# Kernel optimization log

Hardware: AMD Instinct MI355X
Metric: run time of the kernel (lower is better)

Reference implementation:

```python
import jax, jax.numpy as jnp
import numpy as np

VOCAB, D, E, B, S = 32000, 1024, 4, 4, 1024
DF = 4 * D  # Expert.internal_dim = d_model * 4


def setup_inputs() -> dict:
    key = jax.random.key(0)
    ks = jax.random.split(key, 14)
    sc = 0.02
    return {
        "tokens": jax.random.randint(ks[0], (B, S), 0, VOCAB),
        "emb": jax.random.normal(ks[1], (VOCAB, D), jnp.float32) * sc,
        "Wih": jax.random.normal(ks[2], (D, D), jnp.float32) * sc,
        "bih": jnp.zeros((D,), jnp.float32),
        "Whh": jax.random.normal(ks[3], (D, D), jnp.float32) * sc,
        "bhh": jnp.zeros((D,), jnp.float32),
        "Wg": jax.random.normal(ks[4], (E, D), jnp.float32) * sc,
        "W1": jax.random.normal(ks[5], (E, D, DF), jnp.float32) * sc,
        "b1": jnp.zeros((E, DF), jnp.float32),
        "W2": jax.random.normal(ks[6], (E, DF, D), jnp.float32) * sc,
        "b2": jnp.zeros((E, D), jnp.float32),
        "Wfc": jax.random.normal(ks[7], (VOCAB, D), jnp.float32) * sc,
        "bfc": jnp.zeros((VOCAB,), jnp.float32),
    }


def reference(tokens, emb, Wih, bih, Whh, bhh, Wg, W1, b1, W2, b2, Wfc, bfc):
    # token embedding: [B,S,D]
    x = emb[tokens]

    # nn.RNN(batch_first=True), tanh nonlinearity, h0 = zeros (h=None path)
    def step(h, xt):
        h = jnp.tanh(xt @ Wih.T + bih + h @ Whh.T + bhh)
        return h, h

    h0 = jnp.zeros((x.shape[0], x.shape[-1]), x.dtype)
    h_last, hs = jax.lax.scan(step, h0, jnp.swapaxes(x, 0, 1))  # hs: [S,B,D]
    x = jnp.swapaxes(hs, 0, 1)  # [B,S,D]

    # DarwinianRouter on pooled sequence repr: softmax gate, top_k=1
    gates = jax.nn.softmax(x.mean(axis=1) @ Wg.T, axis=-1)  # [B,E]
    w, idx = jax.lax.top_k(gates, 1)  # [B,1] each
    idx0 = idx[:, 0]

    # OuroborosMoE dispatch: per-sequence top-1 expert MLP, scaled by gate weight.
    # Gather per-batch expert params instead of boolean-mask gather/scatter loop.
    W1g, b1g = W1[idx0], b1[idx0]          # [B,D,DF], [B,DF]
    W2g, b2g = W2[idx0], b2[idx0]          # [B,DF,D], [B,D]
    h1 = jax.nn.gelu(jnp.einsum('bsd,bdf->bsf', x, W1g) + b1g[:, None, :], approximate=False)
    y = (jnp.einsum('bsf,bfd->bsd', h1, W2g) + b2g[:, None, :]) * w[:, :, None]  # [B,S,D]

    logits = y @ Wfc.T + bfc  # [B,S,VOCAB]
    return logits


if __name__ == "__main__":
    out = reference(**setup_inputs())
    print(out.shape)
```

## Files before the change

### kernel.cpp

```cpp
#include <hip/hip_runtime.h>
#include <hip/hip_bf16.h>
#include <math.h>

#define DD    1024
#define SS    1024
#define BB    4
#define EE    4
#define DFF   4096
#define VOC   32000

typedef __attribute__((ext_vector_type(8))) short v8s;
typedef __attribute__((ext_vector_type(4))) float v4f;

__device__ __forceinline__ unsigned short f2b(float f) {
    unsigned u = __float_as_uint(f);
    unsigned r = (u + 0x7FFFu + ((u >> 16) & 1u)) >> 16;
    return (unsigned short)r;
}
__device__ __forceinline__ float b2f(unsigned short h) {
    return __uint_as_float((unsigned)h << 16);
}

__device__ __forceinline__ void xcd_swizzle(int& bx, int& by) {
    int gx = gridDim.x;
    int nwg = gx * gridDim.y;
    int id = by * gx + bx;
    int q = nwg >> 3, r = nwg & 7;
    int xcd = id & 7, o = id >> 3;
    int swz = (xcd < r ? xcd * (q + 1) : r * (q + 1) + (xcd - r) * q) + o;
    bx = swz % gx; by = swz / gx;
}

template<bool GATHER>
__global__ __launch_bounds__(256)
void split_cast(const float* __restrict__ src, const int* __restrict__ tokens,
                unsigned short* __restrict__ Xhi, unsigned short* __restrict__ Xlo)
{
    const int row = blockIdx.x;
    const float4* s;
    if constexpr (GATHER)
        s = (const float4*)(src + (size_t)tokens[row] * DD);
    else
        s = (const float4*)(src + (size_t)row * DD);
    const int c = threadIdx.x;
    float4 v = s[c];
    ushort4 hi, lo;
    hi.x = f2b(v.x); hi.y = f2b(v.y); hi.z = f2b(v.z); hi.w = f2b(v.w);
    lo.x = f2b(v.x - b2f(hi.x)); lo.y = f2b(v.y - b2f(hi.y));
    lo.z = f2b(v.z - b2f(hi.z)); lo.w = f2b(v.w - b2f(hi.w));
    ((ushort4*)Xhi)[(size_t)row * 256 + c] = hi;
    ((ushort4*)Xlo)[(size_t)row * 256 + c] = lo;
}

__global__ __launch_bounds__(1024)
void rnn_kernel(const float* __restrict__ U,
                const float* __restrict__ Whh,
                unsigned short* __restrict__ HSbf,
                unsigned long long* __restrict__ hpair,
                float* __restrict__ MEANX)
{
    __shared__ float hs_s[2][1088];

    const int tid = threadIdx.x;
    const int b  = blockIdx.x >> 4;
    const int gg = blockIdx.x & 15;
    const int out = tid >> 4;
    const int chunk = tid & 15;
    const int d_own = gg * 64 + out;
    const bool is_res = (chunk == 0);

    const float4* wrow = (const float4*)(Whh + (size_t)d_own * DD + chunk * 64);
    float4 w00 = wrow[0],  w01 = wrow[1],  w02 = wrow[2],  w03 = wrow[3];
    float4 w04 = wrow[4],  w05 = wrow[5],  w06 = wrow[6],  w07 = wrow[7];
    float4 w08 = wrow[8],  w09 = wrow[9],  w10 = wrow[10], w11 = wrow[11];
    float4 w12 = wrow[12], w13 = wrow[13], w14 = wrow[14], w15 = wrow[15];

    const int sofs = tid + ((tid >> 6) << 2);
    const int rofs = chunk * 68;
    unsigned long long* hp_b = hpair + (size_t)b * 2048;

    float m_acc = 0.f;

    for (int t = 0; t < SS; ++t) {
        const int par = t & 1;
        float u_pre = 0.f;
        if (is_res)
            u_pre = U[((size_t)(b * SS + t)) * DD + d_own];

        if (t > 0) {
            const unsigned long long* pp = hp_b + (size_t)((t - 1) & 1) * 1024 + tid;
            uint2 q;
            const unsigned tg = (unsigned)t;
            for (;;) {
                asm volatile(
                    "global_load_dwordx2 %0, %1, off sc0 sc1\n\t"
                    "s_waitcnt vmcnt(0)"
                    : "=&v"(q) : "v"(pp) : "memory");
                if (q.y == tg) break;
                __builtin_amdgcn_s_sleep(1);
            }
            hs_s[par][sofs] = __uint_as_float(q.x);
        }
        __syncthreads();

        float acc = 0.f;
        if (t > 0) {
            const float* rb = &hs_s[par][rofs];
            float4 h;
            h = *(const float4*)(rb +  0); acc += w00.x*h.x + w00.y*h.y + w00.z*h.z + w00.w*h.w;
            h = *(const float4*)(rb +  4); acc += w01.x*h.x + w01.y*h.y + w01.z*h.z + w01.w*h.w;
            h = *(const float4*)(rb +  8); acc += w02.x*h.x + w02.y*h.y + w02.z*h.z + w02.w*h.w;
            h = *(const float4*)(rb + 12); acc += w03.x*h.x + w03.y*h.y + w03.z*h.z + w03.w*h.w;
            h = *(const float4*)(rb + 16); acc += w04.x*h.x + w04.y*h.y + w04.z*h.z + w04.w*h.w;
            h = *(const float4*)(rb + 20); acc += w05.x*h.x + w05.y*h.y + w05.z*h.z + w05.w*h.w;
            h = *(const float4*)(rb + 24); acc += w06.x*h.x + w06.y*h.y + w06.z*h.z + w06.w*h.w;
            h = *(const float4*)(rb + 28); acc += w07.x*h.x + w07.y*h.y + w07.z*h.z + w07.w*h.w;
            h = *(const float4*)(rb + 32); acc += w08.x*h.x + w08.y*h.y + w08.z*h.z + w08.w*h.w;
            h = *(const float4*)(rb + 36); acc += w09.x*h.x + w09.y*h.y + w09.z*h.z + w09.w*h.w;
            h = *(const float4*)(rb + 40); acc += w10.x*h.x + w10.y*h.y + w10.z*h.z + w10.w*h.w;
            h = *(const float4*)(rb + 44); acc += w11.x*h.x + w11.y*h.y + w11.z*h.z + w11.w*h.w;
            h = *(const float4*)(rb + 48); acc += w12.x*h.x + w12.y*h.y + w12.z*h.z + w12.w*h.w;
            h = *(const float4*)(rb + 52); acc += w13.x*h.x + w13.y*h.y + w13.z*h.z + w13.w*h.w;
            h = *(const float4*)(rb + 56); acc += w14.x*h.x + w14.y*h.y + w14.z*h.z + w14.w*h.w;
            h = *(const float4*)(rb + 60); acc += w15.x*h.x + w15.y*h.y + w15.z*h.z + w15.w*h.w;
            acc += __shfl_xor(acc, 1);
            acc += __shfl_xor(acc, 2);
            acc += __shfl_xor(acc, 4);
            acc += __shfl_xor(acc, 8);
        }

        if (is_res) {
            float h = tanhf(u_pre + acc);
            HSbf[((size_t)(b * SS + t)) * DD + d_own] = f2b(h);
            m_acc += h;
            unsigned long long pk =
                ((unsigned long long)(unsigned)(t + 1) << 32) |
                (unsigned long long)__float_as_uint(h);
            __hip_atomic_store(hp_b + (size_t)par * 1024 + d_own, pk,
                               __ATOMIC_RELAXED, __HIP_MEMORY_SCOPE_AGENT);
        }
    }

    if (is_res)
        MEANX[b * DD + d_own] = m_acc * (1.0f / (float)SS);
}

__global__ __launch_bounds__(256)
void gate_kernel(const float* __restrict__ MEANX, const float* __restrict__ Wg,
                 float* __restrict__ WGATE, int* __restrict__ IDX)
{
    __shared__ float sc[4][4];
    const int tid = threadIdx.x;
    const int p = tid >> 4, l = tid & 15;
    const int b = p >> 2, e = p & 3;
    float acc = 0.f;
    for (int j = 0; j < 64; ++j)
        acc += MEANX[b * DD + l * 64 + j] * Wg[e * DD + l * 64 + j];
    acc += __shfl_xor(acc, 1); acc += __shfl_xor(acc, 2);
    acc += __shfl_xor(acc, 4); acc += __shfl_xor(acc, 8);
    if (l == 0) sc[b][e] = acc;
    __syncthreads();
    if (tid < 4) {
        float s0 = sc[tid][0], s1 = sc[tid][1], s2 = sc[tid][2], s3 = sc[tid][3];
        float mx = fmaxf(fmaxf(s0, s1), fmaxf(s2, s3));
        float e0 = expf(s0 - mx), e1 = expf(s1 - mx);
        float e2 = expf(s2 - mx), e3 = expf(s3 - mx);
        float inv = 1.0f / (e0 + e1 + e2 + e3);
        float pr[4] = {e0 * inv, e1 * inv, e2 * inv, e3 * inv};
        int arg = 0; float best = pr[0];
        if (pr[1] > best) { best = pr[1]; arg = 1; }
        if (pr[2] > best) { best = pr[2]; arg = 2; }
        if (pr[3] > best) { best = pr[3]; arg = 3; }
        WGATE[tid] = best;
        IDX[tid] = arg;
    }
}

__global__ __launch_bounds__(256)
void cast_kernel(const float* __restrict__ in, unsigned short* __restrict__ out,
                 long long n4)
{
    long long stride = (long long)gridDim.x * blockDim.x;
    for (long long i = (long long)blockIdx.x * blockDim.x + threadIdx.x;
         i < n4; i += stride) {
        float4 v = ((const float4*)in)[i];
        ushort4 o;
        o.x = f2b(v.x); o.y = f2b(v.y); o.z = f2b(v.z); o.w = f2b(v.w);
        ((ushort4*)out)[i] = o;
    }
}

__global__ __launch_bounds__(256)
void transpose_cast(const float* __restrict__ src, const int* __restrict__ expIdx,
                    unsigned short* __restrict__ dst, int R, int C,
                    long long srcExpStride, long long dstZStride)
{
    __shared__ float tbuf[32][33];
    const int tid = threadIdx.x;
    const int z = blockIdx.z;
    const float* S = src + (long long)expIdx[z] * srcExpStride;
    unsigned short* D = dst + (long long)z * dstZStride;
    const int r0 = blockIdx.y * 32, c0 = blockIdx.x * 32;
    const int tr = tid >> 3, tc = (tid & 7) * 4;
    float4 v = *(const float4*)(S + (long long)(r0 + tr) * C + c0 + tc);
    tbuf[tr][tc + 0] = v.x; tbuf[tr][tc + 1] = v.y;
    tbuf[tr][tc + 2] = v.z; tbuf[tr][tc + 3] = v.w;
    __syncthreads();
    ushort4 o;
    o.x = f2b(tbuf[tc + 0][tr]); o.y = f2b(tbuf[tc + 1][tr]);
    o.z = f2b(tbuf[tc + 2][tr]); o.w = f2b(tbuf[tc + 3][tr]);
    *(ushort4*)(D + (long long)(c0 + tr) * R + r0 + tc) = o;
}

__device__ __forceinline__ void load_lds16(const void* g, void* l) {
    __builtin_amdgcn_global_load_lds(
        (const __attribute__((address_space(1))) unsigned int*)g,
        (__attribute__((address_space(3))) unsigned int*)l, 16, 0, 0);
}

template<int EPI>
__global__ __launch_bounds__(256)
void gemm_bf16(const unsigned short* __restrict__ A,
               const unsigned short* __restrict__ Bt,
               const float* __restrict__ bias,
               void* __restrict__ Cv,
               int N, int K,
               long long aStride, long long cStride, long long btStride,
               const float* __restrict__ scaleP, const int* __restrict__ expIdx)
{
    __shared__ __align__(16) unsigned short Asm[128 * 32];
    __shared__ __align__(16) unsigned short Bsm[128 * 32];

    const int tid = threadIdx.x;
    const int wave = tid >> 6, lane = tid & 63;
    int bxs = blockIdx.x, bys = blockIdx.y;
    xcd_swizzle(bxs, bys);
    const int bm = bys * 128, bn = bxs * 128;
    const int bz = blockIdx.z;
    const int wm = (wave >> 1) * 64, wn = (wave & 1) * 64;
    const int fr = lane & 15, kh = lane >> 4;

    const unsigned short* Az  = A  + (long long)bz * aStride;
    const unsigned short* Btz = Bt + (long long)bz * btStride;
    const float* bp = bias + (expIdx ? (long long)expIdx[bz] * N : 0);

    const int lo0 = wave * 1024 + lane * 16;
    const int lo1 = 4096 + lo0;
    const int r0 = lo0 >> 6, q0 = (lo0 & 63) >> 1;
    const int r1 = lo1 >> 6, q1 = (lo1 & 63) >> 1;
    const unsigned short* a0 = Az  + (size_t)(bm + r0) * K + q0;
    const unsigned short* a1 = Az  + (size_t)(bm + r1) * K + q1;
    const unsigned short* b0 = Btz + (size_t)(bn + r0) * K + q0;
    const unsigned short* b1 = Btz + (size_t)(bn + r1) * K + q1;

    v4f acc[4][4];
    #pragma unroll
    for (int i = 0; i < 4; ++i)
        #pragma unroll
        for (int j = 0; j < 4; ++j) {
            acc[i][j][0] = 0.f; acc[i][j][1] = 0.f;
            acc[i][j][2] = 0.f; acc[i][j][3] = 0.f;
        }

    for (int k0 = 0; k0 < K; k0 += 32) {
        load_lds16(a0 + k0, (char*)Asm + wave * 1024);
        load_lds16(a1 + k0, (char*)Asm + 4096 + wave * 1024);
        load_lds16(b0 + k0, (char*)Bsm + wave * 1024);
        load_lds16(b1 + k0, (char*)Bsm + 4096 + wave * 1024);
        __syncthreads();

        v8s af[4], bfv[4];
        #pragma unroll
        for (int f = 0; f < 4; ++f) {
            af[f]  = *(const v8s*)((const char*)Asm + ((wm + f * 16 + fr) << 6) + (kh << 4));
            bfv[f] = *(const v8s*)((const char*)Bsm + ((wn + f * 16 + fr) << 6) + (kh << 4));
        }
        #pragma unroll
        for (int fi = 0; fi < 4; ++fi)
            #pragma unroll
            for (int fj = 0; fj < 4; ++fj)
                acc[fi][fj] = __builtin_amdgcn_mfma_f32_16x16x32_bf16(
                    af[fi], bfv[fj], acc[fi][fj], 0, 0, 0);
        __syncthreads();
    }

    const float scale = (EPI == 2) ? scaleP[bz] : 1.0f;
    #pragma unroll
    for (int fi = 0; fi < 4; ++fi) {
        #pragma unroll
        for (int fj = 0; fj < 4; ++fj) {
            v4f t = acc[fi][fj];
            int col = bn + wn + fj * 16 + fr;
            float bb = bp[col];
            int rbase = bm + wm + fi * 16 + (kh << 2);
            #pragma unroll
            for (int r = 0; r < 4; ++r) {
                float v = t[r] + bb;
                if constexpr (EPI == 1)
                    v = 0.5f * v * (1.0f + erff(v * 0.70710678118654752440f));
                if constexpr (EPI == 2)
                    v *= scale;
                size_t off = (size_t)bz * (size_t)cStride +
                             (size_t)(rbase + r) * N + col;
                if constexpr (EPI == 0)
                    ((float*)Cv)[off] = v;
                else
                    ((unsigned short*)Cv)[off] = f2b(v);
            }
        }
    }
}

__global__ __launch_bounds__(256)
void gemm_bf16_split(const unsigned short* __restrict__ Ahi,
                     const unsigned short* __restrict__ Alo,
                     const unsigned short* __restrict__ Bhi,
                     const unsigned short* __restrict__ Blo,
                     const float* __restrict__ bias1,
                     const float* __restrict__ bias2,
                     float* __restrict__ C, int N, int K)
{
    __shared__ __align__(16) unsigned short AsmH[128 * 32];
    __shared__ __align__(16) unsigned short AsmL[128 * 32];
    __shared__ __align__(16) unsigned short BsmH[128 * 32];
    __shared__ __align__(16) unsigned short BsmL[128 * 32];

    const int tid = threadIdx.x;
    const int wave = tid >> 6, lane = tid & 63;
    int bxs = blockIdx.x, bys = blockIdx.y;
    xcd_swizzle(bxs, bys);
    const int bm = bys * 128, bn = bxs * 128;
    const int wm = (wave >> 1) * 64, wn = (wave & 1) * 64;
    const int fr = lane & 15, kh = lane >> 4;

    const int lo0 = wave * 1024 + lane * 16;
    const int lo1 = 4096 + lo0;
    const int r0 = lo0 >> 6, q0 = (lo0 & 63) >> 1;
    const int r1 = lo1 >> 6, q1 = (lo1 & 63) >> 1;
    const unsigned short* ah0 = Ahi + (size_t)(bm + r0) * K + q0;
    const unsigned short* ah1 = Ahi + (size_t)(bm + r1) * K + q1;
    const unsigned short* al0 = Alo + (size_t)(bm + r0) * K + q0;
    const unsigned short* al1 = Alo + (size_t)(bm + r1) * K + q1;
    const unsigned short* bh0 = Bhi + (size_t)(bn + r0) * K + q0;
    const unsigned short* bh1 = Bhi + (size_t)(bn + r1) * K + q1;
    const unsigned short* bl0 = Blo + (size_t)(bn + r0) * K + q0;
    const unsigned short* bl1 = Blo + (size_t)(bn + r1) * K + q1;

    v4f acc[4][4];
    #pragma unroll
    for (int i = 0; i < 4; ++i)
        #pragma unroll
        for (int j = 0; j < 4; ++j) {
            acc[i][j][0] = 0.f; acc[i][j][1] = 0.f;
            acc[i][j][2] = 0.f; acc[i][j][3] = 0.f;
        }

    for (int k0 = 0; k0 < K; k0 += 32) {
        load_lds16(ah0 + k0, (char*)AsmH + wave * 1024);
        load_lds16(ah1 + k0, (char*)AsmH + 4096 + wave * 1024);
        load_lds16(al0 + k0, (char*)AsmL + wave * 1024);
        load_lds16(al1 + k0, (char*)AsmL + 4096 + wave * 1024);
        load_lds16(bh0 + k0, (char*)BsmH + wave * 1024);
        load_lds16(bh1 + k0, (char*)BsmH + 4096 + wave * 1024);
        load_lds16(bl0 + k0, (char*)BsmL + wave * 1024);
        load_lds16(bl1 + k0, (char*)BsmL + 4096 + wave * 1024);
        __syncthreads();

        v8s ahf[4], alf[4];
        #pragma unroll
        for (int f = 0; f < 4; ++f) {
            int ao = ((wm + f * 16 + fr) << 6) + (kh << 4);
            ahf[f] = *(const v8s*)((const char*)AsmH + ao);
            alf[f] = *(const v8s*)((const char*)AsmL + ao);
        }
        #pragma unroll
        for (int fj = 0; fj < 4; ++fj) {
            int bo = ((wn + fj * 16 + fr) << 6) + (kh << 4);
            v8s bh = *(const v8s*)((const char*)BsmH + bo);
            v8s bl = *(const v8s*)((const char*)BsmL + bo);
            #pragma unroll
            for (int fi = 0; fi < 4; ++fi) {
                acc[fi][fj] = __builtin_amdgcn_mfma_f32_16x16x32_bf16(
                    alf[fi], bh, acc[fi][fj], 0, 0, 0);
                acc[fi][fj] = __builtin_amdgcn_mfma_f32_16x16x32_bf16(
                    ahf[fi], bl, acc[fi][fj], 0, 0, 0);
                acc[fi][fj] = __builtin_amdgcn_mfma_f32_16x16x32_bf16(
                    ahf[fi], bh, acc[fi][fj], 0, 0, 0);
            }
        }
        __syncthreads();
    }

    #pragma unroll
    for (int fi = 0; fi < 4; ++fi) {
        #pragma unroll
        for (int fj = 0; fj < 4; ++fj) {
            v4f t = acc[fi][fj];
            int col = bn + wn + fj * 16 + fr;
            float bb = bias1[col] + bias2[col];
            int rbase = bm + wm + fi * 16 + (kh << 2);
            #pragma unroll
            for (int r = 0; r < 4; ++r)
                C[(size_t)(rbase + r) * N + col] = t[r] + bb;
        }
    }
}

extern "C" void kernel_launch(void* const* d_in, const int* in_sizes, int n_in,
                              void* d_out, int out_size, void* d_ws, size_t ws_size,
                              hipStream_t stream)
{
    const int*   tokens = (const int*)  d_in[0];
    const float* emb    = (const float*)d_in[1];
    const float* Wih    = (const float*)d_in[2];
    const float* bih    = (const float*)d_in[3];
    const float* Whh    = (const float*)d_in[4];
    const float* bhh    = (const float*)d_in[5];
    const float* Wg     = (const float*)d_in[6];
    const float* W1     = (const float*)d_in[7];
    const float* b1     = (const float*)d_in[8];
    const float* W2     = (const float*)d_in[9];
    const float* b2     = (const float*)d_in[10];
    const float* Wfc    = (const float*)d_in[11];
    const float* bfc    = (const float*)d_in[12];
    float* out = (float*)d_out;
    float* ws  = (float*)d_ws;

    float*          U     = ws;
    float*          HSdead= ws + 4194304;
    unsigned short* HSbf  = (unsigned short*)(ws + 8388608);
    float*          Ebase = ws + 10485760;
    float*          Fbase = ws + 18874368;
    unsigned short* Ybf   = (unsigned short*)(ws + 27262976);
    float*          MEANX = ws + 29360128;
    float*          WGATE = ws + 29364224;
    int*            IDX   = (int*)(ws + 29364228);
    unsigned long long* HPAIR = (unsigned long long*)HSdead;
    unsigned short* Xhi   = (unsigned short*)Ebase;
    unsigned short* Xlo   = (unsigned short*)(Ebase + 2097152);
    unsigned short* Whi   = (unsigned short*)(Ebase + 4194304);
    unsigned short* Wlo   = (unsigned short*)(Ebase + 4718592);
    unsigned short* W1T   = (unsigned short*)Ebase;
    unsigned short* W2T   = (unsigned short*)Ebase;
    unsigned short* H1bf  = (unsigned short*)Fbase;
    unsigned short* Wfcbf = (unsigned short*)Ebase;

    hipMemsetAsync(HPAIR, 0, (size_t)BB * 2 * 1024 * sizeof(unsigned long long),
                   stream);

    split_cast<true ><<<BB * SS, 256, 0, stream>>>(emb, tokens, Xhi, Xlo);
    split_cast<false><<<DD, 256, 0, stream>>>(Wih, nullptr, Whi, Wlo);

    gemm_bf16_split<<<dim3(DD / 128, (BB * SS) / 128, 1), 256, 0, stream>>>(
        Xhi, Xlo, Whi, Wlo, bih, bhh, U, DD, DD);

    rnn_kernel<<<64, 1024, 0, stream>>>(U, Whh, HSbf, HPAIR, MEANX);

    gate_kernel<<<1, 256, 0, stream>>>(MEANX, Wg, WGATE, IDX);

    transpose_cast<<<dim3(DFF / 32, DD / 32, BB), 256, 0, stream>>>(
        W1, IDX, W1T, DD, DFF, (long long)DD * DFF, (long long)DFF * DD);

    gemm_bf16<1><<<dim3(DFF / 128, SS / 128, BB), 256, 0, stream>>>(
        HSbf, W1T, b1, H1bf, DFF, DD,
        (long long)SS * DD, (long long)SS * DFF, (long long)DFF * DD,
        nullptr, IDX);

    transpose_cast<<<dim3(DD / 32, DFF / 32, BB), 256, 0, stream>>>(
        W2, IDX, W2T, DFF, DD, (long long)DFF * DD, (long long)DD * DFF);

    gemm_bf16<2><<<dim3(DD / 128, SS / 128, BB), 256, 0, stream>>>(
        H1bf, W2T, b2, Ybf, DD, DFF,
        (long long)SS * DFF, (long long)SS * DD, (long long)DD * DFF,
        WGATE, IDX);

    cast_kernel<<<4096, 256, 0, stream>>>(Wfc, Wfcbf, (long long)VOC * DD / 4);

    gemm_bf16<0><<<dim3(VOC / 128, (BB * SS) / 128, 1), 256, 0, stream>>>(
        Ybf, Wfcbf, bfc, out, VOC, DD, 0, 0, 0, nullptr, nullptr);
}
```

Baseline: 2.784 ms.

## Spread RNN recurrence over 256 workgroups with 16 outputs each

The persistent RNN kernel now launches 256 workgroups instead of 64. Each workgroup owns 16 hidden outputs, one per 64-lane wavefront, and each lane does a 16-element dot product followed by a full-wavefront shuffle reduction. This cuts per-thread serial work and register-held weights per timestep and spreads the recurrence over more CUs. In exchange, four times as many workgroups must poll the global handshake each step, adding cross-CU synchronisation traffic. It also relies on all 256 workgroups being co-resident to avoid deadlock, which the launch bound of 4 is meant to support.

```diff
diff --git a/kernel.cpp b/kernel.cpp
--- a/kernel.cpp
+++ b/kernel.cpp
@@ -11,6 +11,7 @@
 
 typedef __attribute__((ext_vector_type(8))) short v8s;
 typedef __attribute__((ext_vector_type(4))) float v4f;
+typedef __attribute__((ext_vector_type(4))) float f32x4;
 
 __device__ __forceinline__ unsigned short f2b(float f) {
     unsigned u = __float_as_uint(f);
@@ -52,31 +53,33 @@
     ((ushort4*)Xlo)[(size_t)row * 256 + c] = lo;
 }
 
-__global__ __launch_bounds__(1024)
+__global__ __launch_bounds__(1024, 4)
 void rnn_kernel(const float* __restrict__ U,
                 const float* __restrict__ Whh,
                 unsigned short* __restrict__ HSbf,
                 unsigned long long* __restrict__ hpair,
                 float* __restrict__ MEANX)
 {
-    __shared__ float hs_s[2][1088];
+    __shared__ __align__(16) float hs_s[2][1280];
 
     const int tid = threadIdx.x;
-    const int b  = blockIdx.x >> 4;
-    const int gg = blockIdx.x & 15;
-    const int out = tid >> 4;
-    const int chunk = tid & 15;
-    const int d_own = gg * 64 + out;
-    const bool is_res = (chunk == 0);
-
-    const float4* wrow = (const float4*)(Whh + (size_t)d_own * DD + chunk * 64);
-    float4 w00 = wrow[0],  w01 = wrow[1],  w02 = wrow[2],  w03 = wrow[3];
-    float4 w04 = wrow[4],  w05 = wrow[5],  w06 = wrow[6],  w07 = wrow[7];
-    float4 w08 = wrow[8],  w09 = wrow[9],  w10 = wrow[10], w11 = wrow[11];
-    float4 w12 = wrow[12], w13 = wrow[13], w14 = wrow[14], w15 = wrow[15];
-
-    const int sofs = tid + ((tid >> 6) << 2);
-    const int rofs = chunk * 68;
+    const int b  = blockIdx.x >> 6;
+    const int gg = blockIdx.x & 63;
+    const int w  = tid >> 6;
+    const int l  = tid & 63;
+    const int d_own = gg * 16 + w;
+    const bool is_res = (l == 0);
+
+    const float* wrow = Whh + (size_t)d_own * DD + l * 16;
+    f32x4 w0, w1, w2, w3;
+    asm volatile("global_load_dwordx4 %0, %1, off"           : "=v"(w0) : "v"(wrow) : "memory");
+    asm volatile("global_load_dwordx4 %0, %1, off offset:16" : "=v"(w1) : "v"(wrow) : "memory");
+    asm volatile("global_load_dwordx4 %0, %1, off offset:32" : "=v"(w2) : "v"(wrow) : "memory");
+    asm volatile("global_load_dwordx4 %0, %1, off offset:48" : "=v"(w3) : "v"(wrow) : "memory");
+    asm volatile("s_waitcnt vmcnt(0)" ::: "memory");
+
+    const int sofs = tid + ((tid >> 4) << 2);
+    const int rofs = l * 20;
     unsigned long long* hp_b = hpair + (size_t)b * 2048;
 
     float m_acc = 0.f;
@@ -106,27 +109,20 @@
         float acc = 0.f;
         if (t > 0) {
             const float* rb = &hs_s[par][rofs];
-            float4 h;
-            h = *(const float4*)(rb +  0); acc += w00.x*h.x + w00.y*h.y + w00.z*h.z + w00.w*h.w;
-            h = *(const float4*)(rb +  4); acc += w01.x*h.x + w01.y*h.y + w01.z*h.z + w01.w*h.w;
-            h = *(const float4*)(rb +  8); acc += w02.x*h.x + w02.y*h.y + w02.z*h.z + w02.w*h.w;
-            h = *(const float4*)(rb + 12); acc += w03.x*h.x + w03.y*h.y + w03.z*h.z + w03.w*h.w;
-            h = *(const float4*)(rb + 16); acc += w04.x*h.x + w04.y*h.y + w04.z*h.z + w04.w*h.w;
-            h = *(const float4*)(rb + 20); acc += w05.x*h.x + w05.y*h.y + w05.z*h.z + w05.w*h.w;
-            h = *(const float4*)(rb + 24); acc += w06.x*h.x + w06.y*h.y + w06.z*h.z + w06.w*h.w;
-            h = *(const float4*)(rb + 28); acc += w07.x*h.x + w07.y*h.y + w07.z*h.z + w07.w*h.w;
-            h = *(const float4*)(rb + 32); acc += w08.x*h.x + w08.y*h.y + w08.z*h.z + w08.w*h.w;
-            h = *(const float4*)(rb + 36); acc += w09.x*h.x + w09.y*h.y + w09.z*h.z + w09.w*h.w;
-            h = *(const float4*)(rb + 40); acc += w10.x*h.x + w10.y*h.y + w10.z*h.z + w10.w*h.w;
-            h = *(const float4*)(rb + 44); acc += w11.x*h.x + w11.y*h.y + w11.z*h.z + w11.w*h.w;
-            h = *(const float4*)(rb + 48); acc += w12.x*h.x + w12.y*h.y + w12.z*h.z + w12.w*h.w;
-            h = *(const float4*)(rb + 52); acc += w13.x*h.x + w13.y*h.y + w13.z*h.z + w13.w*h.w;
-            h = *(const float4*)(rb + 56); acc += w14.x*h.x + w14.y*h.y + w14.z*h.z + w14.w*h.w;
-            h = *(const float4*)(rb + 60); acc += w15.x*h.x + w15.y*h.y + w15.z*h.z + w15.w*h.w;
+            f32x4 h0 = *(const f32x4*)(rb +  0);
+            f32x4 h1 = *(const f32x4*)(rb +  4);
+            f32x4 h2 = *(const f32x4*)(rb +  8);
+            f32x4 h3 = *(const f32x4*)(rb + 12);
+            acc  = w0.x*h0.x + w0.y*h0.y + w0.z*h0.z + w0.w*h0.w;
+            acc += w1.x*h1.x + w1.y*h1.y + w1.z*h1.z + w1.w*h1.w;
+            acc += w2.x*h2.x + w2.y*h2.y + w2.z*h2.z + w2.w*h2.w;
+            acc += w3.x*h3.x + w3.y*h3.y + w3.z*h3.z + w3.w*h3.w;
             acc += __shfl_xor(acc, 1);
             acc += __shfl_xor(acc, 2);
             acc += __shfl_xor(acc, 4);
             acc += __shfl_xor(acc, 8);
+            acc += __shfl_xor(acc, 16);
+            acc += __shfl_xor(acc, 32);
         }
 
         if (is_res) {
@@ -454,7 +450,7 @@
     gemm_bf16_split<<<dim3(DD / 128, (BB * SS) / 128, 1), 256, 0, stream>>>(
         Xhi, Xlo, Whi, Wlo, bih, bhh, U, DD, DD);
 
-    rnn_kernel<<<64, 1024, 0, stream>>>(U, Whh, HSbf, HPAIR, MEANX);
+    rnn_kernel<<<256, 1024, 0, stream>>>(U, Whh, HSbf, HPAIR, MEANX);
 
     gate_kernel<<<1, 256, 0, stream>>>(MEANX, Wg, WGATE, IDX);
 
```

Result: no change. 2.768 ms (median of 2 runs) (-0.6%).
